# Optimization experiments

Measured on AMD Instinct MI355X. Metric: run time of the kernel, lower is better.

## Reference

```python
import jax, jax.numpy as jnp
import numpy as np

B, C, G = 8, 64, 65536
IN_DIM, OUT_DIM = 64, 64
SLOPE = 0.1


def setup_inputs() -> dict:
    key = jax.random.key(0)
    ks = jax.random.split(key, 5)
    features = jax.random.normal(ks[0], (B, C, G), dtype=jnp.float32)
    # Conv2d(in*2, out, 1, bias=False) weights, squeezed to [out, in*2]
    W0 = jax.random.normal(ks[1], (OUT_DIM, IN_DIM * 2), dtype=jnp.float32) * (1.0 / np.sqrt(IN_DIM * 2))
    W1 = jax.random.normal(ks[2], (OUT_DIM, OUT_DIM * 2), dtype=jnp.float32) * (1.0 / np.sqrt(OUT_DIM * 2))
    W2 = jax.random.normal(ks[3], (OUT_DIM, OUT_DIM * 2), dtype=jnp.float32) * (1.0 / np.sqrt(OUT_DIM * 2))
    W3 = jax.random.normal(ks[4], (OUT_DIM, OUT_DIM * 2), dtype=jnp.float32) * (1.0 / np.sqrt(OUT_DIM * 2))
    return {"features": features, "W0": W0, "W1": W1, "W2": W2, "W3": W3}


def _layer(x, W):
    # x: [B, C, G]; tile the first group's features and build (x, x - x0)
    x0 = x[:, :, :1]                               # [B, C, 1]
    h = jnp.concatenate([x, x - x0], axis=1)       # [B, 2C, G]
    # 1x1 conv == pointwise linear over channels
    y = jnp.einsum("oc,bcg->bog", W, h)            # [B, O, G]
    return jax.nn.leaky_relu(y, negative_slope=SLOPE)


def reference(features, W0, W1, W2, W3):
    x = features
    for W in (W0, W1, W2, W3):
        x = _layer(x, W)
    return jnp.max(x, axis=-1)                     # [B, O]
```

## Files before the change

kernel.cpp:

```cpp
#include <hip/hip_runtime.h>


#define G_TOT 65536

typedef _Float16 hf2 __attribute__((ext_vector_type(2)));
typedef _Float16 hf4 __attribute__((ext_vector_type(4)));
typedef _Float16 hf8 __attribute__((ext_vector_type(8)));
typedef float float4_ __attribute__((ext_vector_type(4)));

static __device__ __forceinline__ hf2 pkh(float x, float y) {
    return __builtin_bit_cast(hf2, __builtin_amdgcn_cvt_pkrtz(x, y));
}


__global__ __launch_bounds__(256) void ge_prep(
    const float* __restrict__ feat,
    const float* __restrict__ W0, const float* __restrict__ W1,
    const float* __restrict__ W2, const float* __restrict__ W3,
    float* __restrict__ ws)
{
    const int tid = threadIdx.x;
    const int blk = blockIdx.x;
    __shared__ float lw[64][129];
    __shared__ float x0[2][64];

    if (blk == 8) {
        unsigned* maxenc = (unsigned*)(ws + 18432);
        maxenc[tid] = 0u; maxenc[tid + 256] = 0u;
        for (int i = tid; i < 4 * 64 * 64; i += 256) {
            int l = i >> 12, o = (i >> 6) & 63, c = i & 63;
            const float* Wl = (l == 0) ? W0 : (l == 1) ? W1 : (l == 2) ? W2 : W3;
            ws[i] = Wl[o * 128 + c] + Wl[o * 128 + 64 + c];
        }
        return;
    }

    const int b = blk;
    if (tid < 64) x0[0][tid] = feat[(size_t)(b * 64 + tid) * G_TOT];
    float* nbias = ws + 16384;
    for (int l = 0; l < 4; ++l) {
        const float* Wl = (l == 0) ? W0 : (l == 1) ? W1 : (l == 2) ? W2 : W3;
        for (int i = tid; i < 64 * 128; i += 256) lw[i >> 7][i & 127] = Wl[i];
        __syncthreads();
        if (tid < 64) {
            const int o = tid;
            const float* src = x0[l & 1];
            float s1 = 0.f, s2 = 0.f;
            for (int c = 0; c < 64; ++c) {
                float xv = src[c];
                s1 += lw[o][c] * xv;
                s2 += lw[o][64 + c] * xv;
            }
            nbias[b * 256 + l * 64 + o] = -s2;
            x0[(l & 1) ^ 1][o] = fmaxf(s1, 0.1f * s1);
        }
        __syncthreads();
    }
}

__global__ __launch_bounds__(256, 2) void ge_main(
    const float* __restrict__ feat,
    const float* __restrict__ ws_wa,
    const float* __restrict__ nbias,
    unsigned* __restrict__ maxenc)
{
    __shared__ _Float16 lws[16384];
    __shared__ float lbias[256];
    __shared__ float blockmax[4][64];
    const int tid = threadIdx.x;
    const int b = blockIdx.x >> 7;

    for (int gi = tid; gi < 4096; gi += 256) {
        int hi = gi & 1, ln = (gi >> 1) & 63, f = gi >> 7;
        int pr = f & 1, mt = (f >> 1) & 3, l = f >> 3;
        int o = (mt << 4) + (ln & 15);
        int c = (((pr << 1) + hi) << 4) + ((ln >> 4) << 2);
        float4_ wv = *(const float4_*)&ws_wa[((l << 6) + o) * 64 + c];
        union { hf2 h2[2]; hf4 h4; } u;
        u.h2[0] = pkh(wv[0], wv[1]);
        u.h2[1] = pkh(wv[2], wv[3]);
        *(hf4*)&lws[gi << 2] = u.h4;
    }
    lbias[tid] = nbias[(b << 8) + tid];
    __syncthreads();

    const int w = tid >> 6, lane = tid & 63, q = lane >> 4, n = lane & 15;
    const int g0 = ((blockIdx.x & 127) << 9) + (w << 7);
    const float* Xrow = feat + (size_t)b * 64 * G_TOT + (size_t)(q << 2) * G_TOT;
    const hf4 k01 = { (_Float16)0.1f, (_Float16)0.1f, (_Float16)0.1f, (_Float16)0.1f };

    float rmax[4][4];
#pragma unroll
    for (int mt = 0; mt < 4; ++mt)
#pragma unroll
        for (int j = 0; j < 4; ++j) rmax[mt][j] = -__builtin_inff();

    float cur[16];
    {
        int gcol = g0 + n;
#pragma unroll
        for (int kf = 0; kf < 4; ++kf)
#pragma unroll
            for (int r = 0; r < 4; ++r)
                cur[kf * 4 + r] = Xrow[(size_t)((kf << 4) + r) * G_TOT + gcol];
    }

#pragma unroll 1
    for (int nt = 0; nt < 8; ++nt) {
        float nxt[16];
        if (nt < 7) {
            int gcol = g0 + ((nt + 1) << 4) + n;
#pragma unroll
            for (int kf = 0; kf < 4; ++kf)
#pragma unroll
                for (int r = 0; r < 4; ++r)
                    nxt[kf * 4 + r] = Xrow[(size_t)((kf << 4) + r) * G_TOT + gcol];
        }

        hf4 bf[4];
#pragma unroll
        for (int kf = 0; kf < 4; ++kf) {
            union { hf2 h2[2]; hf4 h4; } u;
            u.h2[0] = pkh(cur[kf * 4 + 0], cur[kf * 4 + 1]);
            u.h2[1] = pkh(cur[kf * 4 + 2], cur[kf * 4 + 3]);
            bf[kf] = u.h4;
        }

#pragma unroll
        for (int l = 0; l < 4; ++l) {
            float4_ acc[4];
#pragma unroll
            for (int mt = 0; mt < 4; ++mt)
                acc[mt] = *(const float4_*)&lbias[(l << 6) + (mt << 4) + (q << 2)];
#pragma unroll
            for (int mt = 0; mt < 4; ++mt) {
#pragma unroll
                for (int pr = 0; pr < 2; ++pr) {
                    union { hf8 h8; hf4 h4[2]; } ua;
                    ua.h8 = *(const hf8*)&lws[((((((l << 2) + mt) << 1) + pr) << 6) + lane) << 3];
                    acc[mt] = __builtin_amdgcn_mfma_f32_16x16x16f16(ua.h4[0], bf[(pr << 1) + 0], acc[mt], 0, 0, 0);
                    acc[mt] = __builtin_amdgcn_mfma_f32_16x16x16f16(ua.h4[1], bf[(pr << 1) + 1], acc[mt], 0, 0, 0);
                }
            }
            if (l < 3) {
#pragma unroll
                for (int mt = 0; mt < 4; ++mt) {
                    union { hf2 h2[2]; hf4 h4; } u;
                    u.h2[0] = pkh(acc[mt][0], acc[mt][1]);
                    u.h2[1] = pkh(acc[mt][2], acc[mt][3]);
                    hf4 h = u.h4;
                    h = __builtin_elementwise_max(h, h * k01);
                    bf[mt] = h;
                }
            } else {
#pragma unroll
                for (int mt = 0; mt < 4; ++mt)
#pragma unroll
                    for (int j = 0; j < 4; ++j)
                        rmax[mt][j] = fmaxf(rmax[mt][j], acc[mt][j]);
            }
        }
        if (nt < 7) {
#pragma unroll
            for (int i = 0; i < 16; ++i) cur[i] = nxt[i];
        }
    }

#pragma unroll
    for (int mt = 0; mt < 4; ++mt)
#pragma unroll
        for (int j = 0; j < 4; ++j) {
            float v = rmax[mt][j];
            v = fmaxf(v, __shfl_xor(v, 1, 64));
            v = fmaxf(v, __shfl_xor(v, 2, 64));
            v = fmaxf(v, __shfl_xor(v, 4, 64));
            v = fmaxf(v, __shfl_xor(v, 8, 64));
            rmax[mt][j] = fmaxf(v, 0.1f * v);
        }
    if (n == 0) {
#pragma unroll
        for (int mt = 0; mt < 4; ++mt)
#pragma unroll
            for (int j = 0; j < 4; ++j)
                blockmax[w][(mt << 4) + (q << 2) + j] = rmax[mt][j];
    }
    __syncthreads();
    if (tid < 64) {
        float v = fmaxf(fmaxf(blockmax[0][tid], blockmax[1][tid]),
                        fmaxf(blockmax[2][tid], blockmax[3][tid]));
        unsigned s = __float_as_uint(v);
        unsigned enc = (s & 0x80000000u) ? ~s : (s | 0x80000000u);
        atomicMax(&maxenc[b * 64 + tid], enc);
    }
}

__global__ void ge_final(const unsigned* __restrict__ maxenc, float* __restrict__ out)
{
    int i = threadIdx.x;
    if (i < 512) {
        unsigned u = maxenc[i];
        unsigned s = (u & 0x80000000u) ? (u ^ 0x80000000u) : ~u;
        out[i] = __uint_as_float(s);
    }
}

extern "C" void kernel_launch(void* const* d_in, const int* in_sizes, int n_in,
                              void* d_out, int out_size, void* d_ws, size_t ws_size,
                              hipStream_t stream) {
    const float* feat = (const float*)d_in[0];
    const float* W0 = (const float*)d_in[1];
    const float* W1 = (const float*)d_in[2];
    const float* W2 = (const float*)d_in[3];
    const float* W3 = (const float*)d_in[4];
    float* ws = (float*)d_ws;
    unsigned* maxenc = (unsigned*)(ws + 18432);

    ge_prep<<<9, 256, 0, stream>>>(feat, W0, W1, W2, W3, ws);
    ge_main<<<1024, 256, 0, stream>>>(feat, ws, ws + 16384, maxenc);
    ge_final<<<1, 512, 0, stream>>>(maxenc, (float*)d_out);
}
```

Measured before the change: 221.1 us.

## Hold fp16 weight fragments in registers and loop layers outermost over tiles

The prep kernel now writes the summed weights as fp16, already permuted into the MFMA fragment layout, so the main kernel no longer stages weights and bias in LDS. Inside the main kernel, each layer's weight fragments and bias are loaded into registers once. All four 16-column tiles go through that layer before the next one, with activations kept in registers. The grid doubles to 2048 blocks of 64 columns per wave and launch bounds allow 3 blocks per SM, which raises parallelism but drops the double-buffered prefetch of the input and adds register pressure.

```diff
diff --git a/kernel.cpp b/kernel.cpp
--- a/kernel.cpp
+++ b/kernel.cpp
@@ -25,19 +25,24 @@
     __shared__ float x0[2][64];
 
     if (blk == 8) {
-        unsigned* maxenc = (unsigned*)(ws + 18432);
+        unsigned* maxenc = (unsigned*)(ws + 10240);
         maxenc[tid] = 0u; maxenc[tid + 256] = 0u;
-        for (int i = tid; i < 4 * 64 * 64; i += 256) {
-            int l = i >> 12, o = (i >> 6) & 63, c = i & 63;
+        unsigned short* lwsg = (unsigned short*)ws;
+        for (int i = tid; i < 16384; i += 256) {
+            int f = i >> 9, lane = (i >> 3) & 63, e = i & 7;
+            int l = f >> 3, mt = (f >> 1) & 3, pr = f & 1;
+            int o = (mt << 4) + (lane & 15);
+            int c = (((pr << 1) + (e >> 2)) << 4) + ((lane >> 4) << 2) + (e & 3);
             const float* Wl = (l == 0) ? W0 : (l == 1) ? W1 : (l == 2) ? W2 : W3;
-            ws[i] = Wl[o * 128 + c] + Wl[o * 128 + 64 + c];
+            float v = Wl[o * 128 + c] + Wl[o * 128 + 64 + c];
+            lwsg[i] = __builtin_bit_cast(unsigned short, (_Float16)v);
         }
         return;
     }
 
     const int b = blk;
     if (tid < 64) x0[0][tid] = feat[(size_t)(b * 64 + tid) * G_TOT];
-    float* nbias = ws + 16384;
+    float* nbias = ws + 8192;
     for (int l = 0; l < 4; ++l) {
         const float* Wl = (l == 0) ? W0 : (l == 1) ? W1 : (l == 2) ? W2 : W3;
         for (int i = tid; i < 64 * 128; i += 256) lw[i >> 7][i & 127] = Wl[i];
@@ -58,90 +63,78 @@
     }
 }
 
-__global__ __launch_bounds__(256, 2) void ge_main(
+__global__ __launch_bounds__(256, 3) void ge_main(
     const float* __restrict__ feat,
-    const float* __restrict__ ws_wa,
+    const _Float16* __restrict__ lwsg,
     const float* __restrict__ nbias,
     unsigned* __restrict__ maxenc)
 {
-    __shared__ _Float16 lws[16384];
-    __shared__ float lbias[256];
     __shared__ float blockmax[4][64];
     const int tid = threadIdx.x;
-    const int b = blockIdx.x >> 7;
-
-    for (int gi = tid; gi < 4096; gi += 256) {
-        int hi = gi & 1, ln = (gi >> 1) & 63, f = gi >> 7;
-        int pr = f & 1, mt = (f >> 1) & 3, l = f >> 3;
-        int o = (mt << 4) + (ln & 15);
-        int c = (((pr << 1) + hi) << 4) + ((ln >> 4) << 2);
-        float4_ wv = *(const float4_*)&ws_wa[((l << 6) + o) * 64 + c];
-        union { hf2 h2[2]; hf4 h4; } u;
-        u.h2[0] = pkh(wv[0], wv[1]);
-        u.h2[1] = pkh(wv[2], wv[3]);
-        *(hf4*)&lws[gi << 2] = u.h4;
-    }
-    lbias[tid] = nbias[(b << 8) + tid];
-    __syncthreads();
-
+    const int b = blockIdx.x >> 8;
     const int w = tid >> 6, lane = tid & 63, q = lane >> 4, n = lane & 15;
-    const int g0 = ((blockIdx.x & 127) << 9) + (w << 7);
+    const int g0 = ((blockIdx.x & 255) << 8) + (w << 6);
     const float* Xrow = feat + (size_t)b * 64 * G_TOT + (size_t)(q << 2) * G_TOT;
+    const float* nb = nbias + (b << 8);
     const hf4 k01 = { (_Float16)0.1f, (_Float16)0.1f, (_Float16)0.1f, (_Float16)0.1f };
 
+    hf4 actr[4][4];
     float rmax[4][4];
 #pragma unroll
     for (int mt = 0; mt < 4; ++mt)
 #pragma unroll
         for (int j = 0; j < 4; ++j) rmax[mt][j] = -__builtin_inff();
 
-    float cur[16];
-    {
-        int gcol = g0 + n;
-#pragma unroll
-        for (int kf = 0; kf < 4; ++kf)
-#pragma unroll
-            for (int r = 0; r < 4; ++r)
-                cur[kf * 4 + r] = Xrow[(size_t)((kf << 4) + r) * G_TOT + gcol];
-    }
-
-#pragma unroll 1
-    for (int nt = 0; nt < 8; ++nt) {
-        float nxt[16];
-        if (nt < 7) {
-            int gcol = g0 + ((nt + 1) << 4) + n;
-#pragma unroll
-            for (int kf = 0; kf < 4; ++kf)
-#pragma unroll
-                for (int r = 0; r < 4; ++r)
-                    nxt[kf * 4 + r] = Xrow[(size_t)((kf << 4) + r) * G_TOT + gcol];
-        }
-
-        hf4 bf[4];
-#pragma unroll
-        for (int kf = 0; kf < 4; ++kf) {
-            union { hf2 h2[2]; hf4 h4; } u;
-            u.h2[0] = pkh(cur[kf * 4 + 0], cur[kf * 4 + 1]);
-            u.h2[1] = pkh(cur[kf * 4 + 2], cur[kf * 4 + 3]);
-            bf[kf] = u.h4;
-        }
-
-#pragma unroll
-        for (int l = 0; l < 4; ++l) {
+#pragma unroll
+    for (int l = 0; l < 4; ++l) {
+        hf8 wf[4][2];
+#pragma unroll
+        for (int mt = 0; mt < 4; ++mt)
+#pragma unroll
+            for (int pr = 0; pr < 2; ++pr)
+                wf[mt][pr] = *(const hf8*)&lwsg[((((l << 2) + mt) << 1) + pr) * 512 + (lane << 3)];
+        float4_ bias4[4];
+#pragma unroll
+        for (int mt = 0; mt < 4; ++mt)
+            bias4[mt] = *(const float4_*)&nb[(l << 6) + (mt << 4) + (q << 2)];
+
+#pragma unroll
+        for (int t = 0; t < 4; ++t) {
+            hf4 bf[4];
+            if (l == 0) {
+                const int gcol = g0 + (t << 4) + n;
+                float cv[16];
+#pragma unroll
+                for (int kf = 0; kf < 4; ++kf)
+#pragma unroll
+                    for (int r = 0; r < 4; ++r)
+                        cv[kf * 4 + r] = Xrow[(size_t)((kf << 4) + r) * G_TOT + gcol];
+#pragma unroll
+                for (int kf = 0; kf < 4; ++kf) {
+                    union { hf2 h2[2]; hf4 h4; } u;
+                    u.h2[0] = pkh(cv[kf * 4 + 0], cv[kf * 4 + 1]);
+                    u.h2[1] = pkh(cv[kf * 4 + 2], cv[kf * 4 + 3]);
+                    bf[kf] = u.h4;
+                }
+            } else {
+#pragma unroll
+                for (int kf = 0; kf < 4; ++kf) bf[kf] = actr[t][kf];
+            }
+
             float4_ acc[4];
 #pragma unroll
-            for (int mt = 0; mt < 4; ++mt)
-                acc[mt] = *(const float4_*)&lbias[(l << 6) + (mt << 4) + (q << 2)];
-#pragma unroll
             for (int mt = 0; mt < 4; ++mt) {
-#pragma unroll
-                for (int pr = 0; pr < 2; ++pr) {
-                    union { hf8 h8; hf4 h4[2]; } ua;
-                    ua.h8 = *(const hf8*)&lws[((((((l << 2) + mt) << 1) + pr) << 6) + lane) << 3];
-                    acc[mt] = __builtin_amdgcn_mfma_f32_16x16x16f16(ua.h4[0], bf[(pr << 1) + 0], acc[mt], 0, 0, 0);
-                    acc[mt] = __builtin_amdgcn_mfma_f32_16x16x16f16(ua.h4[1], bf[(pr << 1) + 1], acc[mt], 0, 0, 0);
-                }
-            }
+                union { hf8 h8; hf4 h4[2]; } ua0, ua1;
+                ua0.h8 = wf[mt][0];
+                ua1.h8 = wf[mt][1];
+                float4_ a = bias4[mt];
+                a = __builtin_amdgcn_mfma_f32_16x16x16f16(ua0.h4[0], bf[0], a, 0, 0, 0);
+                a = __builtin_amdgcn_mfma_f32_16x16x16f16(ua0.h4[1], bf[1], a, 0, 0, 0);
+                a = __builtin_amdgcn_mfma_f32_16x16x16f16(ua1.h4[0], bf[2], a, 0, 0, 0);
+                a = __builtin_amdgcn_mfma_f32_16x16x16f16(ua1.h4[1], bf[3], a, 0, 0, 0);
+                acc[mt] = a;
+            }
+
             if (l < 3) {
 #pragma unroll
                 for (int mt = 0; mt < 4; ++mt) {
@@ -150,7 +143,7 @@
                     u.h2[1] = pkh(acc[mt][2], acc[mt][3]);
                     hf4 h = u.h4;
                     h = __builtin_elementwise_max(h, h * k01);
-                    bf[mt] = h;
+                    actr[t][mt] = h;
                 }
             } else {
 #pragma unroll
@@ -159,10 +152,6 @@
                     for (int j = 0; j < 4; ++j)
                         rmax[mt][j] = fmaxf(rmax[mt][j], acc[mt][j]);
             }
-        }
-        if (nt < 7) {
-#pragma unroll
-            for (int i = 0; i < 16; ++i) cur[i] = nxt[i];
         }
     }
 
@@ -213,9 +202,9 @@
     const float* W2 = (const float*)d_in[3];
     const float* W3 = (const float*)d_in[4];
     float* ws = (float*)d_ws;
-    unsigned* maxenc = (unsigned*)(ws + 18432);
+    unsigned* maxenc = (unsigned*)(ws + 10240);
 
     ge_prep<<<9, 256, 0, stream>>>(feat, W0, W1, W2, W3, ws);
-    ge_main<<<1024, 256, 0, stream>>>(feat, ws, ws + 16384, maxenc);
+    ge_main<<<2048, 256, 0, stream>>>(feat, (const _Float16*)ws, ws + 8192, maxenc);
     ge_final<<<1, 512, 0, stream>>>(maxenc, (float*)d_out);
 }
```

New measurement: 223.6 us. About the same (+1.1%).
